# Performance work log

Hardware: AMD Instinct MI355X
Metric: run time of the kernel (lower is better)

Reference implementation:

```python
import jax, jax.numpy as jnp
import numpy as np

N = 100000   # nodes
E = 1600000  # edges
IN = 128     # in_dim
H = 64       # hidden_dim
EPS = 1e-5


def layer_norm(x, g, b):
    mu = x.mean(-1, keepdims=True)
    v = ((x - mu) ** 2).mean(-1, keepdims=True)
    return (x - mu) * jax.lax.rsqrt(v + EPS) * g + b


def gcn_conv(x, W, b, src, dst, dinv):
    # PyG GCNConv: x' = D^{-1/2}(A+I)D^{-1/2} X W + b (degrees include self-loops)
    h = x @ W                                   # [N, H]
    coef = dinv[src] * dinv[dst]                # [E]
    agg = jax.ops.segment_sum(h[src] * coef[:, None], dst, num_segments=N)
    agg = agg + h * (dinv * dinv)[:, None]      # self-loop term
    return agg + b


def setup_inputs() -> dict:
    key = jax.random.key(0)
    ks = jax.random.split(key, 12)
    inp = {
        "x": jax.random.normal(ks[0], (N, IN), jnp.float32),
        "edge_index": jax.random.randint(ks[1], (2, E), 0, N, dtype=jnp.int64
                                         if jax.config.jax_enable_x64 else jnp.int32),
    }
    dims = [(IN, H), (H, H), (H, H)]
    for i, (di, do) in enumerate(dims, start=1):
        inp[f"W{i}"] = jax.random.normal(ks[2 * i], (di, do), jnp.float32) / np.sqrt(di)
        inp[f"b{i}"] = jnp.zeros((do,), jnp.float32)
        inp[f"g{i}"] = jnp.ones((do,), jnp.float32)
        inp[f"be{i}"] = jnp.zeros((do,), jnp.float32)
    inp["Wh"] = jax.random.normal(ks[11], (H, 1), jnp.float32) / np.sqrt(H)
    inp["bh"] = jnp.zeros((1,), jnp.float32)
    return inp


def reference(x, edge_index, W1, b1, g1, be1, W2, b2, g2, be2, W3, b3, g3, be3, Wh, bh):
    src, dst = edge_index[0], edge_index[1]
    deg = jax.ops.segment_sum(jnp.ones((E,), x.dtype), dst, num_segments=N) + 1.0
    dinv = jax.lax.rsqrt(deg)
    for W, b, g, be in ((W1, b1, g1, be1), (W2, b2, g2, be2), (W3, b3, g3, be3)):
        x = gcn_conv(x, W, b, src, dst, dinv)
        x = layer_norm(x, g, be)
        x = jax.nn.gelu(x, approximate=False)  # F.gelu default = exact erf
        # dropout omitted (eval mode / deterministic reference)
    return (x @ Wh + bh).squeeze(-1)  # [N]
```

## Files before the change

### kernel.cpp

```cpp
#include <hip/hip_runtime.h>
#include <math.h>

#define NODES 100000
#define EDGES 1600000
#define NBUCK 196
#define BCAP2 12288
#define EPB 4096
#define BINB 391
#define GEMMB 1563
#define G1 782

typedef __attribute__((ext_vector_type(8))) short short8;
typedef __attribute__((ext_vector_type(4))) float floatx4;
typedef __attribute__((ext_vector_type(4))) unsigned uv4;

__device__ __forceinline__ float gsum8(float x) {
#pragma unroll
  for (int o = 4; o > 0; o >>= 1) x += __shfl_xor(x, o, 64);
  return x;
}

__device__ __forceinline__ short f2bf(float f) {
  union { float f; unsigned u; } v;
  v.f = f;
  unsigned r = 0x7fffu + ((v.u >> 16) & 1u);
  return (short)((v.u + r) >> 16);
}
__device__ __forceinline__ float bflo(unsigned p) {
  union { unsigned u; float f; } v; v.u = p << 16; return v.f;
}
__device__ __forceinline__ float bfhi(unsigned p) {
  union { unsigned u; float f; } v; v.u = p & 0xffff0000u; return v.f;
}

__device__ __forceinline__ void bin_body(char* smemraw, int b, const int* __restrict__ src,
                                         const int* __restrict__ dst, int* __restrict__ bins,
                                         int* __restrict__ gcur) {
  int* cnt = (int*)smemraw;
  int* gbase = cnt + NBUCK;
  int* lcur = gbase + NBUCK;
  int t = threadIdx.x;
  for (int i = t; i < NBUCK; i += 256) cnt[i] = 0;
  __syncthreads();
  int base = b * EPB;
  int s[16], d[16];
#pragma unroll
  for (int j = 0; j < 16; ++j) {
    int e = base + j * 256 + t;
    if (e < EDGES) {
      s[j] = src[e];
      d[j] = dst[e];
      atomicAdd(&cnt[d[j] >> 9], 1);
    } else {
      d[j] = -1;
    }
  }
  __syncthreads();
  for (int i = t; i < NBUCK; i += 256) {
    int c = cnt[i];
    gbase[i] = c ? atomicAdd(&gcur[i], c) : 0;
    lcur[i] = 0;
  }
  __syncthreads();
#pragma unroll
  for (int j = 0; j < 16; ++j) {
    if (d[j] >= 0) {
      int bk = d[j] >> 9;
      int lp = atomicAdd(&lcur[bk], 1);
      int pos = gbase[bk] + lp;
      if (pos < BCAP2) bins[bk * BCAP2 + pos] = s[j] | ((d[j] & 511) << 17);
    }
  }
}

__device__ __forceinline__ void fill_body(char* smemraw, int b, const int* __restrict__ bins,
                                          const int* __restrict__ gcur, int* __restrict__ rowptr,
                                          float* __restrict__ dinv, int* __restrict__ csr) {
  int* bsm = (int*)smemraw;
  int* cnt = bsm + 256;
  int* cur = cnt + 512;
  int* wtot = cur + 512;
  int t = threadIdx.x;
  int v = 0;
  if (t < NBUCK) { v = gcur[t]; if (v > BCAP2) v = BCAP2; }
  bsm[t] = v;
  cnt[t] = 0; cnt[t + 256] = 0;
  __syncthreads();
  for (int o = 1; o < 256; o <<= 1) {
    int u = (t >= o) ? bsm[t - o] : 0;
    __syncthreads();
    bsm[t] += u;
    __syncthreads();
  }
  if (b == 0 && t == NBUCK - 1) rowptr[NODES] = bsm[t];
  int cb = gcur[b]; if (cb > BCAP2) cb = BCAP2;
  int base = bsm[b] - cb;
  const int* bp = &bins[(size_t)b * BCAP2];
  for (int i = t; i < cb; i += 256)
    atomicAdd(&cnt[(bp[i] >> 17) & 511], 1);
  __syncthreads();
  int a0 = cnt[2 * t], a1 = cnt[2 * t + 1];
  int sum2 = a0 + a1;
  int lane = t & 63, w = t >> 6;
  int inc = sum2;
#pragma unroll
  for (int o = 1; o < 64; o <<= 1) {
    int u = __shfl_up(inc, o, 64);
    if (lane >= o) inc += u;
  }
  if (lane == 63) wtot[w] = inc;
  __syncthreads();
  int wpre = 0;
  for (int ww = 0; ww < w; ++ww) wpre += wtot[ww];
  int r0 = base + wpre + inc - sum2;
  int r1 = r0 + a0;
  int n0 = b * 512 + 2 * t, n1 = n0 + 1;
  if (n0 < NODES) { rowptr[n0] = r0; dinv[n0] = rsqrtf((float)a0 + 1.0f); }
  if (n1 < NODES) { rowptr[n1] = r1; dinv[n1] = rsqrtf((float)a1 + 1.0f); }
  cur[2 * t] = r0; cur[2 * t + 1] = r1;
  __syncthreads();
  for (int i = t; i < cb; i += 256) {
    int pk = bp[i];
    int p = atomicAdd(&cur[(pk >> 17) & 511], 1);
    csr[p] = pk & 0x1FFFF;
  }
}

__device__ __forceinline__ void gemm_body(char* smemraw, int tile0, const float* __restrict__ x,
                                          const float* __restrict__ W, short* __restrict__ hs) {
  constexpr int K = 128, KP = K + 8;
  short* wt = (short*)smemraw;
  for (int idx = threadIdx.x; idx < K * 64; idx += 256) {
    int k = idx >> 6, n = idx & 63;
    wt[n * KP + k] = f2bf(W[idx]);
  }
  __syncthreads();
  int wid = threadIdx.x >> 6, lane = threadIdx.x & 63;
  int tile = tile0 + wid;
  if (tile * 16 >= NODES) return;
  int m = lane & 15, q = lane >> 4;

  short8 bfr[4][K / 32];
#pragma unroll
  for (int ct = 0; ct < 4; ++ct)
#pragma unroll
    for (int ks = 0; ks < K / 32; ++ks)
      bfr[ct][ks] = *reinterpret_cast<const short8*>(&wt[(ct * 16 + m) * KP + ks * 32 + q * 8]);

  floatx4 acc[4];
#pragma unroll
  for (int ct = 0; ct < 4; ++ct) acc[ct] = {0.f, 0.f, 0.f, 0.f};
  int r0 = tile * 16;
#pragma unroll
  for (int ks = 0; ks < K / 32; ++ks) {
    const float* xp = &x[(size_t)(r0 + m) * K + ks * 32 + q * 8];
    floatx4 a0 = *reinterpret_cast<const floatx4*>(xp);
    floatx4 a1 = *reinterpret_cast<const floatx4*>(xp + 4);
    short8 af;
#pragma unroll
    for (int j = 0; j < 4; ++j) { af[j] = f2bf(a0[j]); af[4 + j] = f2bf(a1[j]); }
#pragma unroll
    for (int ct = 0; ct < 4; ++ct)
      acc[ct] = __builtin_amdgcn_mfma_f32_16x16x32_bf16(af, bfr[ct][ks], acc[ct], 0, 0, 0);
  }
#pragma unroll
  for (int ct = 0; ct < 4; ++ct)
#pragma unroll
    for (int r = 0; r < 4; ++r) {
      int row = r0 + q * 4 + r, col = ct * 16 + m;
      hs[row * 64 + col] = f2bf(acc[ct][r]);
    }
}

__device__ __forceinline__ void prepw_body(int p, const float* __restrict__ W2,
                                           const float* __restrict__ W3,
                                           short* __restrict__ wt2, short* __restrict__ wt3) {
  const float* W = (p < 4) ? W2 : W3;
  short* wt = (p < 4) ? wt2 : wt3;
  int b0 = (p & 3) * 1024;
  for (int i = threadIdx.x; i < 1024; i += 256) {
    int e = b0 + i;
    int k = e >> 6, n = e & 63;
    wt[n * 72 + k] = f2bf(W[e]);
  }
}

__device__ __forceinline__ void acc8(float acc[8], const uv4 (&v)[8], const float (&wj)[8]) {
#pragma unroll
  for (int j = 0; j < 8; ++j)
#pragma unroll
    for (int w = 0; w < 4; ++w) {
      acc[2 * w]     += wj[j] * bflo(v[j][w]);
      acc[2 * w + 1] += wj[j] * bfhi(v[j][w]);
    }
}

template <bool PRESCALED>
__device__ __forceinline__ void do_agg(const uv4* __restrict__ hsv, const float* __restrict__ dinv,
                                       const int* __restrict__ csr, int n, int e0, int e1,
                                       int lane, float dn, float acc[8]) {
  int q = lane & 7, srcb = lane & 0x38;
  uv4 sv = hsv[(size_t)n * 8 + q];
#pragma unroll
  for (int w = 0; w < 4; ++w) {
    float lo = bflo(sv[w]), hi = bfhi(sv[w]);
    if constexpr (PRESCALED) { acc[2 * w] = lo; acc[2 * w + 1] = hi; }
    else { acc[2 * w] = lo * dn; acc[2 * w + 1] = hi * dn; }
  }
  int deg = e1 - e0;
  if (deg <= 0) return;
  int p0 = e0 + q, p1 = p0 + 8, p2 = p0 + 16, p3 = p0 + 24;
  int i0 = csr[p0 < e1 ? p0 : e0];
  int i1 = csr[p1 < e1 ? p1 : e0];
  int i2 = csr[p2 < e1 ? p2 : e0];
  int i3 = csr[p3 < e1 ? p3 : e0];
  float g0 = 1.0f, g1 = 1.0f, g2 = 1.0f, g3 = 1.0f;
  if constexpr (!PRESCALED) { g0 = dinv[i0]; g1 = dinv[i1]; g2 = dinv[i2]; g3 = dinv[i3]; }
  int cA = min(deg, 8);
  int cB = min(max(deg - 8, 0), 8);
  int cC = min(max(deg - 16, 0), 8);
  int cD = min(max(deg - 24, 0), 8);
  int sA[8], sB[8], sC[8], sD[8];
#pragma unroll
  for (int j = 0; j < 8; ++j) {
    sA[j] = __shfl(i0, srcb | j, 64);
    sB[j] = __shfl(i1, srcb | j, 64);
  }
  uv4 vA[8], vB[8];
#pragma unroll
  for (int j = 0; j < 8; ++j) vA[j] = hsv[(size_t)sA[j] * 8 + q];
#pragma unroll
  for (int j = 0; j < 8; ++j) vB[j] = hsv[(size_t)sB[j] * 8 + q];
  float wA[8], wB[8], wC[8], wD[8];
#pragma unroll
  for (int j = 0; j < 8; ++j) {
    float bA = 1.0f, bB = 1.0f;
    if constexpr (!PRESCALED) { bA = __shfl(g0, srcb | j, 64); bB = __shfl(g1, srcb | j, 64); }
    wA[j] = (j < cA) ? bA : 0.0f;
    wB[j] = (j < cB) ? bB : 0.0f;
  }
#pragma unroll
  for (int j = 0; j < 8; ++j) {
    sC[j] = __shfl(i2, srcb | j, 64);
    sD[j] = __shfl(i3, srcb | j, 64);
    float bC = 1.0f, bD = 1.0f;
    if constexpr (!PRESCALED) { bC = __shfl(g2, srcb | j, 64); bD = __shfl(g3, srcb | j, 64); }
    wC[j] = (j < cC) ? bC : 0.0f;
    wD[j] = (j < cD) ? bD : 0.0f;
  }
  acc8(acc, vA, wA);
  uv4 vC[8];
#pragma unroll
  for (int j = 0; j < 8; ++j) vC[j] = hsv[(size_t)sC[j] * 8 + q];
  acc8(acc, vB, wB);
  uv4 vD[8];
#pragma unroll
  for (int j = 0; j < 8; ++j) vD[j] = hsv[(size_t)sD[j] * 8 + q];
  acc8(acc, vC, wC);
  acc8(acc, vD, wD);
  if (deg > 32) {
    for (int base = e0 + 32; base < e1; base += 8) {
      int cnt = e1 - base;
      if (cnt > 8) cnt = 8;
      int a = base + (q < cnt ? q : 0);
      int sidx = csr[a];
      float gq = 1.0f;
      if constexpr (!PRESCALED) gq = dinv[sidx];
      int s[8]; float wj[8];
#pragma unroll
      for (int j = 0; j < 8; ++j) {
        s[j] = __shfl(sidx, srcb | j, 64);
        float bj = 1.0f;
        if constexpr (!PRESCALED) bj = __shfl(gq, srcb | j, 64);
        wj[j] = (j < cnt) ? bj : 0.0f;
      }
      uv4 v[8];
#pragma unroll
      for (int j = 0; j < 8; ++j) v[j] = hsv[(size_t)s[j] * 8 + q];
      acc8(acc, v, wj);
    }
  }
}

template <bool PRESCALED>
__global__ __launch_bounds__(256) void k_aggg(const short* __restrict__ hs,
                                              const float* __restrict__ dinv,
                                              const int* __restrict__ rowptr,
                                              const int* __restrict__ csr,
                                              const float* __restrict__ bias,
                                              const float* __restrict__ gam,
                                              const float* __restrict__ bet,
                                              const short* __restrict__ wtg,
                                              short* __restrict__ hsn) {
  __shared__ __align__(16) short wt[64 * 72];
  __shared__ __align__(16) short ut[32 * 72];
  int t = threadIdx.x;
  {
    const int* wp = (const int*)wtg;
    int* wd = (int*)wt;
    for (int idx = t; idx < 2304; idx += 256) wd[idx] = wp[idx];
  }
  const uv4* hsv = (const uv4*)hs;
  int lane = t & 63, wid = t >> 6;
  int g = lane >> 3, q = lane & 7;
  int nb0 = blockIdx.x * 32;
  int r = wid * 8 + g;
  int n = nb0 + r;
  int e0 = rowptr[n], e1 = rowptr[n + 1];
  float dn = dinv[n];
  float acc[8];
  do_agg<PRESCALED>(hsv, dinv, csr, n, e0, e1, lane, dn, acc);

  const floatx4* bi4 = (const floatx4*)bias;
  floatx4 b0 = bi4[q * 2], b1 = bi4[q * 2 + 1];
#pragma unroll
  for (int f = 0; f < 4; ++f) { acc[f] = acc[f] * dn + b0[f]; acc[f + 4] = acc[f + 4] * dn + b1[f]; }

  float lsum = 0.f;
#pragma unroll
  for (int f = 0; f < 8; ++f) lsum += acc[f];
  float mu = gsum8(lsum) * (1.0f / 64.0f);
  float d[8], lvar = 0.f;
#pragma unroll
  for (int f = 0; f < 8; ++f) { d[f] = acc[f] - mu; lvar += d[f] * d[f]; }
  float rs = rsqrtf(gsum8(lvar) * (1.0f / 64.0f) + 1e-5f);
  const floatx4* gm4 = (const floatx4*)gam;
  const floatx4* bt4 = (const floatx4*)bet;
  floatx4 g0 = gm4[q * 2], g1 = gm4[q * 2 + 1];
  floatx4 t0 = bt4[q * 2], t1 = bt4[q * 2 + 1];
  short8 us;
#pragma unroll
  for (int f = 0; f < 8; ++f) {
    float gv = (f < 4) ? g0[f] : g1[f - 4];
    float tv = (f < 4) ? t0[f] : t1[f - 4];
    float vv = d[f] * rs * gv + tv;
    float u = 0.5f * vv * (1.0f + erff(vv * 0.70710678118654752f));
    us[f] = f2bf(u * dn);
  }
  *reinterpret_cast<short8*>(&ut[r * 72 + q * 8]) = us;
  __syncthreads();

  int m = lane & 15, q2 = lane >> 4;
  int tile = wid >> 1, cb = (wid & 1) * 2;
  short8 bfr[2][2];
#pragma unroll
  for (int ct = 0; ct < 2; ++ct)
#pragma unroll
    for (int ks = 0; ks < 2; ++ks)
      bfr[ct][ks] = *reinterpret_cast<const short8*>(&wt[((cb + ct) * 16 + m) * 72 + ks * 32 + q2 * 8]);
  floatx4 ac[2];
#pragma unroll
  for (int ct = 0; ct < 2; ++ct) ac[ct] = {0.f, 0.f, 0.f, 0.f};
#pragma unroll
  for (int ks = 0; ks < 2; ++ks) {
    short8 af = *reinterpret_cast<const short8*>(&ut[(tile * 16 + m) * 72 + ks * 32 + q2 * 8]);
#pragma unroll
    for (int ct = 0; ct < 2; ++ct)
      ac[ct] = __builtin_amdgcn_mfma_f32_16x16x32_bf16(af, bfr[ct][ks], ac[ct], 0, 0, 0);
  }
#pragma unroll
  for (int ct = 0; ct < 2; ++ct)
#pragma unroll
    for (int rr = 0; rr < 4; ++rr) {
      int row = nb0 + tile * 16 + q2 * 4 + rr, col = (cb + ct) * 16 + m;
      hsn[row * 64 + col] = f2bf(ac[ct][rr]);
    }
}

__global__ __launch_bounds__(256) void k_agg_fin(const short* __restrict__ hs,
                                                 const float* __restrict__ dinv,
                                                 const int* __restrict__ rowptr,
                                                 const int* __restrict__ csr,
                                                 const float* __restrict__ bias,
                                                 const float* __restrict__ gam,
                                                 const float* __restrict__ bet,
                                                 const float* __restrict__ Wh,
                                                 const float* __restrict__ bh,
                                                 float* __restrict__ out) {
  const uv4* hsv = (const uv4*)hs;
  int lane = threadIdx.x & 63, wid = threadIdx.x >> 6;
  int g = lane >> 3, q = lane & 7;
  int n = blockIdx.x * 32 + wid * 8 + g;
  int e0 = rowptr[n], e1 = rowptr[n + 1];
  float dn = dinv[n];
  float acc[8];
  do_agg<true>(hsv, dinv, csr, n, e0, e1, lane, dn, acc);
  const floatx4* bi4 = (const floatx4*)bias;
  floatx4 b0 = bi4[q * 2], b1 = bi4[q * 2 + 1];
#pragma unroll
  for (int f = 0; f < 4; ++f) { acc[f] = acc[f] * dn + b0[f]; acc[f + 4] = acc[f + 4] * dn + b1[f]; }
  float lsum = 0.f;
#pragma unroll
  for (int f = 0; f < 8; ++f) lsum += acc[f];
  float mu = gsum8(lsum) * (1.0f / 64.0f);
  float d[8], lvar = 0.f;
#pragma unroll
  for (int f = 0; f < 8; ++f) { d[f] = acc[f] - mu; lvar += d[f] * d[f]; }
  float rs = rsqrtf(gsum8(lvar) * (1.0f / 64.0f) + 1e-5f);
  const floatx4* gm4 = (const floatx4*)gam;
  const floatx4* bt4 = (const floatx4*)bet;
  floatx4 g0 = gm4[q * 2], g1 = gm4[q * 2 + 1];
  floatx4 t0 = bt4[q * 2], t1 = bt4[q * 2 + 1];
  const floatx4* wh4 = (const floatx4*)Wh;
  floatx4 w0 = wh4[q * 2], w1 = wh4[q * 2 + 1];
  float lp = 0.f;
#pragma unroll
  for (int f = 0; f < 8; ++f) {
    float gv = (f < 4) ? g0[f] : g1[f - 4];
    float tv = (f < 4) ? t0[f] : t1[f - 4];
    float wv = (f < 4) ? w0[f] : w1[f - 4];
    float vv = d[f] * rs * gv + tv;
    float u = 0.5f * vv * (1.0f + erff(vv * 0.70710678118654752f));
    lp += u * wv;
  }
  float p = gsum8(lp);
  if (q == 0) out[n] = p + bh[0];
}

__global__ __launch_bounds__(256) void k_pre1(const int* __restrict__ src, const int* __restrict__ dst,
                                              int* __restrict__ bins, int* __restrict__ gcur,
                                              const float* __restrict__ x, const float* __restrict__ W1,
                                              short* __restrict__ hs,
                                              const float* __restrict__ W2, const float* __restrict__ W3,
                                              short* __restrict__ wt2, short* __restrict__ wt3) {
  __shared__ __align__(16) char smem[64 * 136 * 2];
  int b = blockIdx.x;
  if (b < BINB) bin_body(smem, b, src, dst, bins, gcur);
  else if (b < BINB + G1) gemm_body(smem, (b - BINB) * 4, x, W1, hs);
  else prepw_body(b - BINB - G1, W2, W3, wt2, wt3);
}

__global__ __launch_bounds__(256) void k_pre2(const int* __restrict__ bins, const int* __restrict__ gcur,
                                              int* __restrict__ rowptr, float* __restrict__ dinv,
                                              int* __restrict__ csr,
                                              const float* __restrict__ x, const float* __restrict__ W1,
                                              short* __restrict__ hs) {
  __shared__ __align__(16) char smem[64 * 136 * 2];
  int b = blockIdx.x;
  if (b < NBUCK) fill_body(smem, b, bins, gcur, rowptr, dinv, csr);
  else gemm_body(smem, (G1 + (b - NBUCK)) * 4, x, W1, hs);
}

__global__ __launch_bounds__(256) void k_bin2(const int* src, const int* dst, int* bins, int* gcur) {
  __shared__ __align__(16) char smem[64 * 136 * 2];
  bin_body(smem, blockIdx.x, src, dst, bins, gcur);
}
__global__ __launch_bounds__(256) void k_fillb2(const int* bins, const int* gcur, int* rowptr,
                                                float* dinv, int* csr) {
  __shared__ __align__(16) char smem[64 * 136 * 2];
  fill_body(smem, blockIdx.x, bins, gcur, rowptr, dinv, csr);
}
__global__ __launch_bounds__(256) void k_gemm(const float* x, const float* W, short* hs) {
  __shared__ __align__(16) char smem[64 * 136 * 2];
  gemm_body(smem, blockIdx.x * 4, x, W, hs);
}
__global__ __launch_bounds__(256) void k_prepw(const float* W2, const float* W3, short* wt2, short* wt3) {
  prepw_body(blockIdx.x, W2, W3, wt2, wt3);
}

extern "C" void kernel_launch(void* const* d_in, const int* in_sizes, int n_in,
                              void* d_out, int out_size, void* d_ws, size_t ws_size,
                              hipStream_t stream) {
  const float* x  = (const float*)d_in[0];
  const int* ei   = (const int*)d_in[1];
  const float* W1 = (const float*)d_in[2];
  const float* b1 = (const float*)d_in[3];
  const float* g1 = (const float*)d_in[4];
  const float* be1= (const float*)d_in[5];
  const float* W2 = (const float*)d_in[6];
  const float* b2 = (const float*)d_in[7];
  const float* g2 = (const float*)d_in[8];
  const float* be2= (const float*)d_in[9];
  const float* W3 = (const float*)d_in[10];
  const float* b3 = (const float*)d_in[11];
  const float* g3 = (const float*)d_in[12];
  const float* be3= (const float*)d_in[13];
  const float* Wh = (const float*)d_in[14];
  const float* bh = (const float*)d_in[15];
  const int* srcp = ei;
  const int* dstp = ei + EDGES;

  char* ws = (char*)d_ws;
  size_t off = 0;
  auto take = [&](size_t bytes) {
    char* p = ws + off;
    off = (off + bytes + 255) & ~(size_t)255;
    return p;
  };
  float* dinv = (float*)take((size_t)NODES * 4);
  int* rowptr = (int*)take((size_t)(NODES + 1) * 4);
  int* csr    = (int*)take((size_t)EDGES * 4);
  short* hs_a = (short*)take((size_t)NODES * 64 * 2);
  short* hs_b = (short*)take((size_t)NODES * 64 * 2);
  short* wt2  = (short*)take((size_t)64 * 72 * 2);
  short* wt3  = (short*)take((size_t)64 * 72 * 2);

  size_t bins_sz = (size_t)NBUCK * BCAP2 * 4;
  bool overlap = (ws_size >= off + bins_sz + 4096);
  int* bins; int* gcur;
  if (overlap) {
    bins = (int*)take(bins_sz);
    gcur = (int*)take((size_t)NBUCK * 4);
  } else {
    bins = (int*)hs_a;
    gcur = (int*)hs_b;
  }

  (void)hipMemsetAsync(gcur, 0, (size_t)NBUCK * 4, stream);
  if (overlap) {
    k_pre1<<<BINB + G1 + 8, 256, 0, stream>>>(srcp, dstp, bins, gcur, x, W1, hs_a, W2, W3, wt2, wt3);
    k_pre2<<<NBUCK + (GEMMB - G1), 256, 0, stream>>>(bins, gcur, rowptr, dinv, csr, x, W1, hs_a);
  } else {
    k_bin2<<<BINB, 256, 0, stream>>>(srcp, dstp, bins, gcur);
    k_fillb2<<<NBUCK, 256, 0, stream>>>(bins, gcur, rowptr, dinv, csr);
    k_gemm<<<GEMMB, 256, 0, stream>>>(x, W1, hs_a);
    k_prepw<<<8, 256, 0, stream>>>(W2, W3, wt2, wt3);
  }
  k_aggg<false><<<NODES / 32, 256, 0, stream>>>(hs_a, dinv, rowptr, csr, b1, g1, be1, wt2, hs_b);
  k_aggg<true><<<NODES / 32, 256, 0, stream>>>(hs_b, dinv, rowptr, csr, b2, g2, be2, wt3, hs_a);
  k_agg_fin<<<NODES / 32, 256, 0, stream>>>(hs_a, dinv, rowptr, csr, b3, g3, be3, Wh, bh, (float*)d_out);
}
```

Baseline: 274.4 us.

## Stage bin and CSR scatters in LDS, move all GEMM1 into pre1, simplify aggregation loop

The binning kernel now sorts each block's edges by bucket in shared memory and writes them out as contiguous runs per bucket. The CSR fill stages each bucket's column indices in LDS and writes them back coalesced, replacing scattered global stores. All first-layer GEMM tiles move into the first pre-kernel, so the second kernel only does the fill. The unrolled 32-edge prefetch in aggregation is replaced by a uniform 8-edge loop, with a multiply-free path for prescaled layers. This trades extra LDS use and barriers for better write coalescing, but it gives up memory-level parallelism in the gather loop.

```diff
diff --git a/kernel.cpp b/kernel.cpp
--- a/kernel.cpp
+++ b/kernel.cpp
@@ -8,7 +8,6 @@
 #define EPB 4096
 #define BINB 391
 #define GEMMB 1563
-#define G1 782
 
 typedef __attribute__((ext_vector_type(8))) short short8;
 typedef __attribute__((ext_vector_type(4))) float floatx4;
@@ -33,16 +32,21 @@
   union { unsigned u; float f; } v; v.u = p & 0xffff0000u; return v.f;
 }
 
+#define BIN_SMEM (4 * 256 * 4 + EPB * 4 + EPB)
 __device__ __forceinline__ void bin_body(char* smemraw, int b, const int* __restrict__ src,
                                          const int* __restrict__ dst, int* __restrict__ bins,
                                          int* __restrict__ gcur) {
   int* cnt = (int*)smemraw;
-  int* gbase = cnt + NBUCK;
-  int* lcur = gbase + NBUCK;
+  int* gb = cnt + 256;
+  int* lb = gb + 256;
+  int* lcur = lb + 256;
+  int* rec = lcur + 256;
+  unsigned char* rbk = (unsigned char*)(rec + EPB);
   int t = threadIdx.x;
-  for (int i = t; i < NBUCK; i += 256) cnt[i] = 0;
+  cnt[t] = 0;
   __syncthreads();
   int base = b * EPB;
+  int nv = EDGES - base; if (nv > EPB) nv = EPB;
   int s[16], d[16];
 #pragma unroll
   for (int j = 0; j < 16; ++j) {
@@ -56,23 +60,39 @@
     }
   }
   __syncthreads();
-  for (int i = t; i < NBUCK; i += 256) {
-    int c = cnt[i];
-    gbase[i] = c ? atomicAdd(&gcur[i], c) : 0;
-    lcur[i] = 0;
-  }
+  int c = cnt[t];
+  lb[t] = c;
+  __syncthreads();
+  for (int o = 1; o < 256; o <<= 1) {
+    int u = (t >= o) ? lb[t - o] : 0;
+    __syncthreads();
+    lb[t] += u;
+    __syncthreads();
+  }
+  int ex = lb[t] - c;
+  gb[t] = (c > 0) ? atomicAdd(&gcur[t], c) : 0;
+  __syncthreads();
+  lb[t] = ex;
+  lcur[t] = ex;
   __syncthreads();
 #pragma unroll
   for (int j = 0; j < 16; ++j) {
     if (d[j] >= 0) {
       int bk = d[j] >> 9;
       int lp = atomicAdd(&lcur[bk], 1);
-      int pos = gbase[bk] + lp;
-      if (pos < BCAP2) bins[bk * BCAP2 + pos] = s[j] | ((d[j] & 511) << 17);
+      rec[lp] = s[j] | ((d[j] & 511) << 17);
+      rbk[lp] = (unsigned char)bk;
     }
   }
-}
-
+  __syncthreads();
+  for (int i = t; i < nv; i += 256) {
+    int bk = rbk[i];
+    int pos = gb[bk] + (i - lb[bk]);
+    if (pos < BCAP2) bins[bk * BCAP2 + pos] = rec[i];
+  }
+}
+
+#define FILL_SMEM (256 * 4 + 512 * 4 + 512 * 4 + 4 * 4 + BCAP2 * 4)
 __device__ __forceinline__ void fill_body(char* smemraw, int b, const int* __restrict__ bins,
                                           const int* __restrict__ gcur, int* __restrict__ rowptr,
                                           float* __restrict__ dinv, int* __restrict__ csr) {
@@ -80,6 +100,7 @@
   int* cnt = bsm + 256;
   int* cur = cnt + 512;
   int* wtot = cur + 512;
+  int* stage = wtot + 4;
   int t = threadIdx.x;
   int v = 0;
   if (t < NBUCK) { v = gcur[t]; if (v > BCAP2) v = BCAP2; }
@@ -94,7 +115,7 @@
   }
   if (b == 0 && t == NBUCK - 1) rowptr[NODES] = bsm[t];
   int cb = gcur[b]; if (cb > BCAP2) cb = BCAP2;
-  int base = bsm[b] - cb;
+  int bbase = bsm[b] - cb;
   const int* bp = &bins[(size_t)b * BCAP2];
   for (int i = t; i < cb; i += 256)
     atomicAdd(&cnt[(bp[i] >> 17) & 511], 1);
@@ -112,20 +133,23 @@
   __syncthreads();
   int wpre = 0;
   for (int ww = 0; ww < w; ++ww) wpre += wtot[ww];
-  int r0 = base + wpre + inc - sum2;
-  int r1 = r0 + a0;
+  int l0 = wpre + inc - sum2;
+  int l1 = l0 + a0;
   int n0 = b * 512 + 2 * t, n1 = n0 + 1;
-  if (n0 < NODES) { rowptr[n0] = r0; dinv[n0] = rsqrtf((float)a0 + 1.0f); }
-  if (n1 < NODES) { rowptr[n1] = r1; dinv[n1] = rsqrtf((float)a1 + 1.0f); }
-  cur[2 * t] = r0; cur[2 * t + 1] = r1;
+  if (n0 < NODES) { rowptr[n0] = bbase + l0; dinv[n0] = rsqrtf((float)a0 + 1.0f); }
+  if (n1 < NODES) { rowptr[n1] = bbase + l1; dinv[n1] = rsqrtf((float)a1 + 1.0f); }
+  cur[2 * t] = l0; cur[2 * t + 1] = l1;
   __syncthreads();
   for (int i = t; i < cb; i += 256) {
     int pk = bp[i];
-    int p = atomicAdd(&cur[(pk >> 17) & 511], 1);
-    csr[p] = pk & 0x1FFFF;
-  }
-}
-
+    int lp = atomicAdd(&cur[(pk >> 17) & 511], 1);
+    stage[lp] = pk & 0x1FFFF;
+  }
+  __syncthreads();
+  for (int i = t; i < cb; i += 256) csr[bbase + i] = stage[i];
+}
+
+#define GEMM_SMEM (64 * 136 * 2)
 __device__ __forceinline__ void gemm_body(char* smemraw, int tile0, const float* __restrict__ x,
                                           const float* __restrict__ W, short* __restrict__ hs) {
   constexpr int K = 128, KP = K + 8;
@@ -185,16 +209,6 @@
   }
 }
 
-__device__ __forceinline__ void acc8(float acc[8], const uv4 (&v)[8], const float (&wj)[8]) {
-#pragma unroll
-  for (int j = 0; j < 8; ++j)
-#pragma unroll
-    for (int w = 0; w < 4; ++w) {
-      acc[2 * w]     += wj[j] * bflo(v[j][w]);
-      acc[2 * w + 1] += wj[j] * bfhi(v[j][w]);
-    }
-}
-
 template <bool PRESCALED>
 __device__ __forceinline__ void do_agg(const uv4* __restrict__ hsv, const float* __restrict__ dinv,
                                        const int* __restrict__ csr, int n, int e0, int e1,
@@ -207,77 +221,48 @@
     if constexpr (PRESCALED) { acc[2 * w] = lo; acc[2 * w + 1] = hi; }
     else { acc[2 * w] = lo * dn; acc[2 * w + 1] = hi * dn; }
   }
-  int deg = e1 - e0;
-  if (deg <= 0) return;
-  int p0 = e0 + q, p1 = p0 + 8, p2 = p0 + 16, p3 = p0 + 24;
-  int i0 = csr[p0 < e1 ? p0 : e0];
-  int i1 = csr[p1 < e1 ? p1 : e0];
-  int i2 = csr[p2 < e1 ? p2 : e0];
-  int i3 = csr[p3 < e1 ? p3 : e0];
-  float g0 = 1.0f, g1 = 1.0f, g2 = 1.0f, g3 = 1.0f;
-  if constexpr (!PRESCALED) { g0 = dinv[i0]; g1 = dinv[i1]; g2 = dinv[i2]; g3 = dinv[i3]; }
-  int cA = min(deg, 8);
-  int cB = min(max(deg - 8, 0), 8);
-  int cC = min(max(deg - 16, 0), 8);
-  int cD = min(max(deg - 24, 0), 8);
-  int sA[8], sB[8], sC[8], sD[8];
-#pragma unroll
-  for (int j = 0; j < 8; ++j) {
-    sA[j] = __shfl(i0, srcb | j, 64);
-    sB[j] = __shfl(i1, srcb | j, 64);
-  }
-  uv4 vA[8], vB[8];
-#pragma unroll
-  for (int j = 0; j < 8; ++j) vA[j] = hsv[(size_t)sA[j] * 8 + q];
-#pragma unroll
-  for (int j = 0; j < 8; ++j) vB[j] = hsv[(size_t)sB[j] * 8 + q];
-  float wA[8], wB[8], wC[8], wD[8];
-#pragma unroll
-  for (int j = 0; j < 8; ++j) {
-    float bA = 1.0f, bB = 1.0f;
-    if constexpr (!PRESCALED) { bA = __shfl(g0, srcb | j, 64); bB = __shfl(g1, srcb | j, 64); }
-    wA[j] = (j < cA) ? bA : 0.0f;
-    wB[j] = (j < cB) ? bB : 0.0f;
-  }
-#pragma unroll
-  for (int j = 0; j < 8; ++j) {
-    sC[j] = __shfl(i2, srcb | j, 64);
-    sD[j] = __shfl(i3, srcb | j, 64);
-    float bC = 1.0f, bD = 1.0f;
-    if constexpr (!PRESCALED) { bC = __shfl(g2, srcb | j, 64); bD = __shfl(g3, srcb | j, 64); }
-    wC[j] = (j < cC) ? bC : 0.0f;
-    wD[j] = (j < cD) ? bD : 0.0f;
-  }
-  acc8(acc, vA, wA);
-  uv4 vC[8];
-#pragma unroll
-  for (int j = 0; j < 8; ++j) vC[j] = hsv[(size_t)sC[j] * 8 + q];
-  acc8(acc, vB, wB);
-  uv4 vD[8];
-#pragma unroll
-  for (int j = 0; j < 8; ++j) vD[j] = hsv[(size_t)sD[j] * 8 + q];
-  acc8(acc, vC, wC);
-  acc8(acc, vD, wD);
-  if (deg > 32) {
-    for (int base = e0 + 32; base < e1; base += 8) {
-      int cnt = e1 - base;
-      if (cnt > 8) cnt = 8;
-      int a = base + (q < cnt ? q : 0);
-      int sidx = csr[a];
-      float gq = 1.0f;
-      if constexpr (!PRESCALED) gq = dinv[sidx];
-      int s[8]; float wj[8];
-#pragma unroll
-      for (int j = 0; j < 8; ++j) {
-        s[j] = __shfl(sidx, srcb | j, 64);
-        float bj = 1.0f;
-        if constexpr (!PRESCALED) bj = __shfl(gq, srcb | j, 64);
+  for (int base = e0; base < e1; base += 8) {
+    int cnt = e1 - base;
+    if (cnt > 8) cnt = 8;
+    int a = base + (q < cnt ? q : 0);
+    int sidx = csr[a];
+    float gq = 1.0f;
+    if constexpr (!PRESCALED) gq = dinv[sidx];
+    int s[8]; float wj[8];
+#pragma unroll
+    for (int j = 0; j < 8; ++j) {
+      s[j] = __shfl(sidx, srcb | j, 64);
+      if constexpr (!PRESCALED) {
+        float bj = __shfl(gq, srcb | j, 64);
         wj[j] = (j < cnt) ? bj : 0.0f;
+      } else {
+        wj[j] = 1.0f;
       }
-      uv4 v[8];
-#pragma unroll
-      for (int j = 0; j < 8; ++j) v[j] = hsv[(size_t)s[j] * 8 + q];
-      acc8(acc, v, wj);
+    }
+    uv4 v[8];
+#pragma unroll
+    for (int j = 0; j < 8; ++j) v[j] = hsv[(size_t)s[j] * 8 + q];
+    if constexpr (PRESCALED) {
+      if (cnt == 8) {
+#pragma unroll
+        for (int j = 0; j < 8; ++j)
+#pragma unroll
+          for (int w = 0; w < 4; ++w) { acc[2 * w] += bflo(v[j][w]); acc[2 * w + 1] += bfhi(v[j][w]); }
+      } else {
+#pragma unroll
+        for (int j = 0; j < 8; ++j)
+          if (j < cnt)
+#pragma unroll
+            for (int w = 0; w < 4; ++w) { acc[2 * w] += bflo(v[j][w]); acc[2 * w + 1] += bfhi(v[j][w]); }
+      }
+    } else {
+#pragma unroll
+      for (int j = 0; j < 8; ++j)
+#pragma unroll
+        for (int w = 0; w < 4; ++w) {
+          acc[2 * w]     += wj[j] * bflo(v[j][w]);
+          acc[2 * w + 1] += wj[j] * bfhi(v[j][w]);
+        }
     }
   }
 }
@@ -423,35 +408,31 @@
                                               short* __restrict__ hs,
                                               const float* __restrict__ W2, const float* __restrict__ W3,
                                               short* __restrict__ wt2, short* __restrict__ wt3) {
-  __shared__ __align__(16) char smem[64 * 136 * 2];
+  __shared__ __align__(16) char smem[BIN_SMEM];
   int b = blockIdx.x;
   if (b < BINB) bin_body(smem, b, src, dst, bins, gcur);
-  else if (b < BINB + G1) gemm_body(smem, (b - BINB) * 4, x, W1, hs);
-  else prepw_body(b - BINB - G1, W2, W3, wt2, wt3);
+  else if (b < BINB + GEMMB) gemm_body(smem, (b - BINB) * 4, x, W1, hs);
+  else prepw_body(b - BINB - GEMMB, W2, W3, wt2, wt3);
 }
 
 __global__ __launch_bounds__(256) void k_pre2(const int* __restrict__ bins, const int* __restrict__ gcur,
                                               int* __restrict__ rowptr, float* __restrict__ dinv,
-                                              int* __restrict__ csr,
-                                              const float* __restrict__ x, const float* __restrict__ W1,
-                                              short* __restrict__ hs) {
-  __shared__ __align__(16) char smem[64 * 136 * 2];
-  int b = blockIdx.x;
-  if (b < NBUCK) fill_body(smem, b, bins, gcur, rowptr, dinv, csr);
-  else gemm_body(smem, (G1 + (b - NBUCK)) * 4, x, W1, hs);
+                                              int* __restrict__ csr) {
+  __shared__ __align__(16) char smem[FILL_SMEM];
+  fill_body(smem, blockIdx.x, bins, gcur, rowptr, dinv, csr);
 }
 
 __global__ __launch_bounds__(256) void k_bin2(const int* src, const int* dst, int* bins, int* gcur) {
-  __shared__ __align__(16) char smem[64 * 136 * 2];
+  __shared__ __align__(16) char smem[BIN_SMEM];
   bin_body(smem, blockIdx.x, src, dst, bins, gcur);
 }
 __global__ __launch_bounds__(256) void k_fillb2(const int* bins, const int* gcur, int* rowptr,
                                                 float* dinv, int* csr) {
-  __shared__ __align__(16) char smem[64 * 136 * 2];
+  __shared__ __align__(16) char smem[FILL_SMEM];
   fill_body(smem, blockIdx.x, bins, gcur, rowptr, dinv, csr);
 }
 __global__ __launch_bounds__(256) void k_gemm(const float* x, const float* W, short* hs) {
-  __shared__ __align__(16) char smem[64 * 136 * 2];
+  __shared__ __align__(16) char smem[GEMM_SMEM];
   gemm_body(smem, blockIdx.x * 4, x, W, hs);
 }
 __global__ __launch_bounds__(256) void k_prepw(const float* W2, const float* W3, short* wt2, short* wt3) {
@@ -508,8 +489,8 @@
 
   (void)hipMemsetAsync(gcur, 0, (size_t)NBUCK * 4, stream);
   if (overlap) {
-    k_pre1<<<BINB + G1 + 8, 256, 0, stream>>>(srcp, dstp, bins, gcur, x, W1, hs_a, W2, W3, wt2, wt3);
-    k_pre2<<<NBUCK + (GEMMB - G1), 256, 0, stream>>>(bins, gcur, rowptr, dinv, csr, x, W1, hs_a);
+    k_pre1<<<BINB + GEMMB + 8, 256, 0, stream>>>(srcp, dstp, bins, gcur, x, W1, hs_a, W2, W3, wt2, wt3);
+    k_pre2<<<NBUCK, 256, 0, stream>>>(bins, gcur, rowptr, dinv, csr);
   } else {
     k_bin2<<<BINB, 256, 0, stream>>>(srcp, dstp, bins, gcur);
     k_fillb2<<<NBUCK, 256, 0, stream>>>(bins, gcur, rowptr, dinv, csr);
```

After: 270.3 us. About the same (-1.5%).
